# Kernel optimization log

Measured on AMD Instinct MI355X. Metric: run time of the kernel, lower is better.

Reference implementation:

```python
import jax, jax.numpy as jnp
import numpy as np

VOCAB, VEC, HID, ATT, DOM, B, S = 50000, 300, 256, 500, 16, 64, 128


def _gru_scan(gi_all, h0, Whh, bhh):
    # gi_all: [S,B,3H] precomputed input projections; returns hs: [S,B,H]
    def step(h, gi):
        gh = h @ Whh.T + bhh
        i_r, i_z, i_n = jnp.split(gi, 3, axis=-1)
        h_r, h_z, h_n = jnp.split(gh, 3, axis=-1)
        r = jax.nn.sigmoid(i_r + h_r)
        zg = jax.nn.sigmoid(i_z + h_z)
        n = jnp.tanh(i_n + r * h_n)
        h_new = (1.0 - zg) * n + zg * h
        return h_new, h_new
    _, hs = jax.lax.scan(step, h0, gi_all)
    return hs


def setup_inputs() -> dict:
    key = jax.random.key(0)
    ks = jax.random.split(key, 16)
    def xavier(k, shape):
        fan_in, fan_out = shape[-1], shape[0]
        std = float(np.sqrt(2.0 / (fan_in + fan_out)))
        return jax.random.normal(k, shape, dtype=jnp.float32) * std
    inp = {
        'x': jax.random.randint(ks[0], (B, S), 0, VOCAB),
        'z': jax.random.randint(ks[1], (B,), 0, DOM),
        'emb': jax.random.normal(ks[2], (VOCAB, VEC), dtype=jnp.float32) * 0.1,
        'Wih_f': xavier(ks[3], (3 * HID, VEC)),
        'Whh_f': xavier(ks[4], (3 * HID, HID)),
        'bih_f': jnp.zeros((3 * HID,), jnp.float32),
        'bhh_f': jnp.zeros((3 * HID,), jnp.float32),
        'Wih_b': xavier(ks[5], (3 * HID, VEC)),
        'Whh_b': xavier(ks[6], (3 * HID, HID)),
        'bih_b': jnp.zeros((3 * HID,), jnp.float32),
        'bhh_b': jnp.zeros((3 * HID,), jnp.float32),
        'att_fc_W': xavier(ks[7], (ATT, 2 * HID)),
        'att_fc_b': jnp.zeros((ATT,), jnp.float32),
        'att_weight': xavier(ks[8], (DOM, ATT)),
        'fc_W': xavier(ks[9], (2, 2 * HID)),
        'fc_b': jnp.zeros((2,), jnp.float32),
    }
    return inp


def reference(x, z, emb, Wih_f, Whh_f, bih_f, bhh_f, Wih_b, Whh_b, bih_b, bhh_b,
              att_fc_W, att_fc_b, att_weight, fc_W, fc_b):
    xe = emb[x]                              # [B,S,VEC]
    xs = jnp.transpose(xe, (1, 0, 2))        # [S,B,VEC] (seq-major like torch GRU)
    h0 = jnp.zeros((x.shape[0], HID), jnp.float32)
    gi_f = jnp.einsum('sbv,gv->sbg', xs, Wih_f) + bih_f
    hs_f = _gru_scan(gi_f, h0, Whh_f, bhh_f)                       # [S,B,H]
    gi_b = jnp.einsum('sbv,gv->sbg', xs[::-1], Wih_b) + bih_b
    hs_b = _gru_scan(gi_b, h0, Whh_b, bhh_b)[::-1]                 # [S,B,H]
    h = jnp.transpose(jnp.concatenate([hs_f, hs_b], axis=-1), (1, 0, 2))  # [B,S,2H]
    hr = jnp.tanh(jnp.einsum('bsh,ah->bsa', h, att_fc_W) + att_fc_b)      # [B,S,ATT]
    # batched gather of per-domain attention vector, then per-row dot
    u = jnp.einsum('bsa,ba->bs', hr, att_weight[z])                        # [B,S]
    att = jax.nn.softmax(u, axis=1)                                        # [B,S]
    pooled = jnp.einsum('bsh,bs->bh', h, att)                              # [B,2H]
    # dropout is identity in eval mode
    return pooled @ fc_W.T + fc_b                                          # [B,2]
```

## Files before the change

kernel.cpp:

```cpp
#include <hip/hip_runtime.h>
#include <math.h>

#define VEC   300
#define HID   256
#define ATT   500
#define NB    64
#define NS    128
#define G3    768
#define GIC   1536
#define H2    512

typedef _Float16 half1;
typedef _Float16 h2_t  __attribute__((ext_vector_type(2)));
typedef _Float16 h4_t  __attribute__((ext_vector_type(4)));
typedef _Float16 f16x8 __attribute__((ext_vector_type(8)));
typedef float    f32x4 __attribute__((ext_vector_type(4)));

#if __has_builtin(__builtin_amdgcn_exp2f)
#define EXP2F(x) __builtin_amdgcn_exp2f(x)
#else
#define EXP2F(x) exp2f(x)
#endif
#if __has_builtin(__builtin_amdgcn_rcpf)
#define RCPF(x) __builtin_amdgcn_rcpf(x)
#else
#define RCPF(x) (1.0f/(x))
#endif

__device__ __forceinline__ float sigm(float x){ return RCPF(1.f + EXP2F(-1.44269504f*x)); }
__device__ __forceinline__ float tanh_fast(float x){ return 1.f - 2.f*RCPF(1.f + EXP2F(2.88539008f*x)); }

#if __has_builtin(__builtin_amdgcn_fdot2)
#define FDOT(w,h,acc) __builtin_amdgcn_fdot2((w),(h),(acc),false)
#else
#define FDOT(w,h,acc) ((acc) + (float)(w).x*(float)(h).x + (float)(w).y*(float)(h).y)
#endif

__global__ __launch_bounds__(256) void k_prep(const float* __restrict__ Wf,
                       const float* __restrict__ Wb, h2_t* __restrict__ Wpk){
  int o = blockIdx.x*256 + threadIdx.x;
  int t = o & 1023;
  int rest = o >> 10;
  int j = rest % 3;
  int p = (rest/3) & 31;
  int dir = rest / 96;
  int u = t & 255, ks = t >> 8;
  const float* W = dir ? Wb : Wf;
  int k0 = ks*64 + 2*p;
  h2_t w;
  w.x = (half1)W[(j*HID+u)*HID + k0];
  w.y = (half1)W[(j*HID+u)*HID + k0 + 1];
  Wpk[o] = w;
}

__global__ __launch_bounds__(256) void k_prepA(const float* __restrict__ afW,
                       half1* __restrict__ afW16){
  int o = blockIdx.x*256 + threadIdx.x;
  int n = o >> 9, k = o & 511;
  afW16[o] = (half1)((n < ATT) ? afW[n*H2 + k] : 0.f);
}

__global__ __launch_bounds__(256)
__attribute__((amdgpu_waves_per_eu(4, 4)))
void k_gi_mfma(const int* __restrict__ x,
      const float* __restrict__ emb,
      const float* __restrict__ Wf, const float* __restrict__ Wb,
      const float* __restrict__ bf, const float* __restrict__ bb,
      float* __restrict__ gi){
  __shared__ half1 Al[128*40];
  __shared__ half1 Bl[128*40];
  __shared__ int   xi[128];
  const int t = threadIdx.x;
  const int row0 = blockIdx.x * 128;
  const int col0 = blockIdx.y * 128;
  if (t < 128) {
    int i = row0 + t; int s = i >> 6; int b = i & 63;
    xi[t] = x[b*NS + s];
  }
  __syncthreads();

  const int lane = t & 63, wid = t >> 6;
  const int wr = wid >> 1, wc = wid & 1;
  const int l15 = lane & 15, lk = lane >> 4;

  f32x4 acc[4][4];
#pragma unroll
  for (int i = 0; i < 4; ++i)
#pragma unroll
    for (int j = 0; j < 4; ++j) acc[i][j] = (f32x4){0.f,0.f,0.f,0.f};

  for (int ks = 0; ks < 10; ++ks) {
#pragma unroll
    for (int l = 0; l < 8; ++l) {
      int idx = l*256 + t;
      int row = idx >> 4;
      int kp  = idx & 15;
      int kk  = ks*32 + kp*2;
      h2_t va; va.x = (half1)0.f; va.y = (half1)0.f;
      h2_t vb; vb.x = (half1)0.f; vb.y = (half1)0.f;
      if (kk < VEC) {
        float2 e = *reinterpret_cast<const float2*>(&emb[(long)xi[row]*VEC + kk]);
        va.x = (half1)e.x; va.y = (half1)e.y;
        int g = col0 + row;
        const float* W = (g < G3) ? &Wf[(long)g*VEC] : &Wb[(long)(g-G3)*VEC];
        float2 w2 = *reinterpret_cast<const float2*>(&W[kk]);
        vb.x = (half1)w2.x; vb.y = (half1)w2.y;
      }
      *reinterpret_cast<h2_t*>(&Al[row*40 + kp*2]) = va;
      *reinterpret_cast<h2_t*>(&Bl[row*40 + kp*2]) = vb;
    }
    __syncthreads();
    f16x8 af[4], bfq[4];
#pragma unroll
    for (int i = 0; i < 4; ++i)
      af[i]  = *reinterpret_cast<const f16x8*>(&Al[(wr*64 + i*16 + l15)*40 + lk*8]);
#pragma unroll
    for (int j = 0; j < 4; ++j)
      bfq[j] = *reinterpret_cast<const f16x8*>(&Bl[(wc*64 + j*16 + l15)*40 + lk*8]);
#pragma unroll
    for (int i = 0; i < 4; ++i)
#pragma unroll
      for (int j = 0; j < 4; ++j)
        acc[i][j] = __builtin_amdgcn_mfma_f32_16x16x32_f16(af[i], bfq[j], acc[i][j], 0, 0, 0);
    __syncthreads();
  }

#pragma unroll
  for (int j = 0; j < 4; ++j) {
    int gcol = col0 + wc*64 + j*16 + l15;
    float bj = (gcol < G3) ? bf[gcol] : bb[gcol - G3];
#pragma unroll
    for (int i = 0; i < 4; ++i) {
      int grow0 = row0 + wr*64 + i*16 + lk*4;
#pragma unroll
      for (int q = 0; q < 4; ++q)
        gi[(long)(grow0 + q)*GIC + gcol] = acc[i][j][q] + bj;
    }
  }
}

#define RP2(M) M(0,1) M(2,3) M(4,5) M(6,7) M(8,9) M(10,11) M(12,13) M(14,15) \
               M(16,17) M(18,19) M(20,21) M(22,23)
#define RPL(M) M(0) M(1) M(2) M(3) M(4) M(5) M(6) M(7) M(8) M(9) M(10) M(11) \
               M(12) M(13) M(14) M(15) M(16) M(17) M(18) M(19) M(20) M(21) M(22) M(23)

__global__ __launch_bounds__(1024)
__attribute__((amdgpu_waves_per_eu(4, 4)))
void k_scan_reg(const float* __restrict__ gi,
     const h2_t* __restrict__ Wpk,
     const float* __restrict__ bhf, const float* __restrict__ bhb,
     float* __restrict__ hseq){
  __shared__ half1 hl16[264];
  __shared__ float part[256*13];
  __shared__ h2_t  lds_w[24*1024];
  const int t   = threadIdx.x;
  const int u   = t & 255;
  const int ks  = t >> 8;
  const int kb  = ks * 64;
  const int dir = blockIdx.x & 1;
  const int b   = blockIdx.x >> 1;
  const float* bhh = dir ? bhb : bhf;
  const h2_t* wp = Wpk + (long)dir*96*1024 + t;

#define DECLW(p) h2_t wA##p, wB##p, wC##p;
  RPL(DECLW)
#define LOADW(p) wA##p = wp[((p)*3+0)*1024]; wB##p = wp[((p)*3+1)*1024]; wC##p = wp[((p)*3+2)*1024];
  RPL(LOADW)
#pragma unroll
  for (int q = 0; q < 24; ++q)
    lds_w[q*1024 + t] = wp[(72+q)*1024];

  float bh0=0.f, bh1=0.f, bh2=0.f;
  if (ks == 0) { bh0 = bhh[u]; bh1 = bhh[HID+u]; bh2 = bhh[2*HID+u]; }
  if (t < 256) hl16[t] = (half1)0.f;
  float hprev = 0.f;
  __syncthreads();

#pragma unroll 1
  for (int tt = 0; tt < NS; ++tt) {
    const int s = dir ? (NS-1-tt) : tt;
    float i0=0.f, i1=0.f, i2=0.f;
    if (ks == 0) {
      long base = ((long)s*NB + b)*GIC + dir*G3 + u;
      i0 = gi[base]; i1 = gi[base+HID]; i2 = gi[base+2*HID];
    }
    float a0=0.f, a1=0.f, a2=0.f;
#define FMAW2(pa,pb) { h4_t hh4 = *reinterpret_cast<const h4_t*>(&hl16[kb + 2*(pa)]); \
    h2_t lo; lo.x = hh4.x; lo.y = hh4.y; \
    h2_t hi; hi.x = hh4.z; hi.y = hh4.w; \
    a0 = FDOT(wA##pa, lo, a0); a1 = FDOT(wB##pa, lo, a1); a2 = FDOT(wC##pa, lo, a2); \
    a0 = FDOT(wA##pb, hi, a0); a1 = FDOT(wB##pb, hi, a1); a2 = FDOT(wC##pb, hi, a2); }
    RP2(FMAW2)
#pragma unroll
    for (int q = 0; q < 4; ++q) {
      h4_t hh4 = *reinterpret_cast<const h4_t*>(&hl16[kb + 48 + 4*q]);
      h2_t lo; lo.x = hh4.x; lo.y = hh4.y;
      h2_t hi; hi.x = hh4.z; hi.y = hh4.w;
      h2_t w0a = lds_w[((2*q)*3+0)*1024 + t];
      h2_t w1a = lds_w[((2*q)*3+1)*1024 + t];
      h2_t w2a = lds_w[((2*q)*3+2)*1024 + t];
      h2_t w0b = lds_w[((2*q+1)*3+0)*1024 + t];
      h2_t w1b = lds_w[((2*q+1)*3+1)*1024 + t];
      h2_t w2b = lds_w[((2*q+1)*3+2)*1024 + t];
      a0 = FDOT(w0a, lo, a0); a1 = FDOT(w1a, lo, a1); a2 = FDOT(w2a, lo, a2);
      a0 = FDOT(w0b, hi, a0); a1 = FDOT(w1b, hi, a1); a2 = FDOT(w2b, hi, a2);
    }
    part[u*13 + ks*3 + 0] = a0;
    part[u*13 + ks*3 + 1] = a1;
    part[u*13 + ks*3 + 2] = a2;
    __syncthreads();
    if (ks == 0) {
      float g0 = bh0 + part[u*13+0] + part[u*13+3] + part[u*13+6] + part[u*13+9];
      float g1 = bh1 + part[u*13+1] + part[u*13+4] + part[u*13+7] + part[u*13+10];
      float g2 = bh2 + part[u*13+2] + part[u*13+5] + part[u*13+8] + part[u*13+11];
      float r  = sigm(i0 + g0);
      float zg = sigm(i1 + g1);
      float n  = tanh_fast(i2 + r*g2);
      float hn = (1.f - zg)*n + zg*hprev;
      hprev = hn;
      hl16[u] = (half1)hn;
      hseq[((long)b*NS + s)*H2 + dir*HID + u] = hn;
    }
    __syncthreads();
  }
}

__global__ __launch_bounds__(256)
__attribute__((amdgpu_waves_per_eu(4, 4)))
void k_att1_mfma(const float* __restrict__ hseq, const half1* __restrict__ afW16,
    const float* __restrict__ afb, const float* __restrict__ attw,
    const int* __restrict__ z, float* __restrict__ ub){
  __shared__ half1 Ah[32*520];
  __shared__ float red[4*32];
  const int t  = threadIdx.x;
  const int b  = blockIdx.x;
  const int s0 = blockIdx.y * 32;
  const int lane = t & 63, w = t >> 6;
  const int l15 = lane & 15, lk = lane >> 4;

#pragma unroll
  for (int l = 0; l < 64; ++l) {
    int idx = l*256 + t;
    int sl = idx >> 9, c = idx & 511;
    Ah[sl*520 + c] = (half1)hseq[((long)b*NS + s0 + sl)*H2 + c];
  }
  __syncthreads();

  f32x4 acc[2][8];
#pragma unroll
  for (int i = 0; i < 2; ++i)
#pragma unroll
    for (int j = 0; j < 8; ++j) acc[i][j] = (f32x4){0.f,0.f,0.f,0.f};

#pragma unroll 2
  for (int ksn = 0; ksn < 16; ++ksn) {
    f16x8 af[2];
#pragma unroll
    for (int mt = 0; mt < 2; ++mt)
      af[mt] = *reinterpret_cast<const f16x8*>(&Ah[(mt*16 + l15)*520 + ksn*32 + lk*8]);
#pragma unroll
    for (int nt = 0; nt < 8; ++nt) {
      int n = w*128 + nt*16 + l15;
      f16x8 bf = *reinterpret_cast<const f16x8*>(&afW16[(long)n*512 + ksn*32 + lk*8]);
#pragma unroll
      for (int mt = 0; mt < 2; ++mt)
        acc[mt][nt] = __builtin_amdgcn_mfma_f32_16x16x32_f16(af[mt], bf, acc[mt][nt], 0, 0, 0);
    }
  }

  float us[8];
#pragma unroll
  for (int i = 0; i < 8; ++i) us[i] = 0.f;
  const int zb = z[b];
#pragma unroll
  for (int nt = 0; nt < 8; ++nt) {
    int n = w*128 + nt*16 + l15;
    float ab = (n < ATT) ? afb[n] : 0.f;
    float aw = (n < ATT) ? attw[zb*ATT + n] : 0.f;
#pragma unroll
    for (int mt = 0; mt < 2; ++mt)
#pragma unroll
      for (int q = 0; q < 4; ++q)
        us[mt*4+q] += tanh_fast(acc[mt][nt][q] + ab) * aw;
  }
#pragma unroll
  for (int off = 1; off < 16; off <<= 1)
#pragma unroll
    for (int i = 0; i < 8; ++i) us[i] += __shfl_xor(us[i], off, 64);
  if (l15 == 0) {
#pragma unroll
    for (int i = 0; i < 8; ++i) {
      int row = (i >> 2)*16 + lk*4 + (i & 3);
      red[w*32 + row] = us[i];
    }
  }
  __syncthreads();
  if (t < 32)
    ub[b*NS + s0 + t] = red[t] + red[32+t] + red[64+t] + red[96+t];
}

__global__ __launch_bounds__(256) void k_att2(const float* __restrict__ hseq,
   const float* __restrict__ ub, const float* __restrict__ fcW,
   const float* __restrict__ fcb, float* __restrict__ out){
  __shared__ float att[NS];
  __shared__ float red[256];
  __shared__ float pool[H2];
  const int t = threadIdx.x, b = blockIdx.x;
  float v = (t < NS) ? ub[b*NS + t] : -3.4e38f;
  red[t] = v; __syncthreads();
  for (int off = 128; off >= 1; off >>= 1) {
    if (t < off) red[t] = fmaxf(red[t], red[t+off]);
    __syncthreads();
  }
  float mx = red[0]; __syncthreads();
  float e = (t < NS) ? EXP2F(1.44269504f*(v - mx)) : 0.f;
  red[t] = e; __syncthreads();
  for (int off = 128; off >= 1; off >>= 1) {
    if (t < off) red[t] += red[t+off];
    __syncthreads();
  }
  float sm = red[0]; __syncthreads();
  if (t < NS) att[t] = e / sm;
  __syncthreads();
#pragma unroll
  for (int rep = 0; rep < 2; ++rep) {
    int c = rep*256 + t;
    float acc = 0.f;
#pragma unroll 4
    for (int s = 0; s < NS; ++s) acc += att[s] * hseq[((long)b*NS + s)*H2 + c];
    pool[c] = acc;
  }
  __syncthreads();
  for (int j = 0; j < 2; ++j) {
    float p = pool[t]*fcW[j*H2+t] + pool[t+256]*fcW[j*H2+t+256];
    red[t] = p; __syncthreads();
    for (int off = 128; off >= 1; off >>= 1) {
      if (t < off) red[t] += red[t+off];
      __syncthreads();
    }
    if (t == 0) out[b*2+j] = red[0] + fcb[j];
    __syncthreads();
  }
}

extern "C" void kernel_launch(void* const* d_in, const int* in_sizes, int n_in,
                              void* d_out, int out_size, void* d_ws, size_t ws_size,
                              hipStream_t stream) {
  const int*   x     = (const int*)  d_in[0];
  const int*   z     = (const int*)  d_in[1];
  const float* emb   = (const float*)d_in[2];
  const float* Wih_f = (const float*)d_in[3];
  const float* Whh_f = (const float*)d_in[4];
  const float* bih_f = (const float*)d_in[5];
  const float* bhh_f = (const float*)d_in[6];
  const float* Wih_b = (const float*)d_in[7];
  const float* Whh_b = (const float*)d_in[8];
  const float* bih_b = (const float*)d_in[9];
  const float* bhh_b = (const float*)d_in[10];
  const float* afW   = (const float*)d_in[11];
  const float* afb   = (const float*)d_in[12];
  const float* attw  = (const float*)d_in[13];
  const float* fcW   = (const float*)d_in[14];
  const float* fcb   = (const float*)d_in[15];

  float* ws    = (float*)d_ws;
  h2_t*  Wpk   = (h2_t*)ws;
  half1* afW16 = (half1*)(ws + 196608);
  float* giW   = ws   + 196608 + 131072;
  float* hseq  = giW  + 12582912;
  float* ubuf  = hseq + 4194304;

  k_prep <<<dim3(768),  dim3(256), 0, stream>>>(Whh_f, Whh_b, Wpk);
  k_prepA<<<dim3(1024), dim3(256), 0, stream>>>(afW, afW16);
  k_gi_mfma<<<dim3(64,12), dim3(256), 0, stream>>>(x, emb, Wih_f, Wih_b, bih_f, bih_b, giW);
  k_scan_reg<<<dim3(128), dim3(1024), 0, stream>>>(giW, Wpk, bhh_f, bhh_b, hseq);
  k_att1_mfma<<<dim3(64,4), dim3(256), 0, stream>>>(hseq, afW16, afb, attw, z, ubuf);
  k_att2<<<dim3(64), dim3(256), 0, stream>>>(hseq, ubuf, fcW, fcb, (float*)d_out);
}
```

Measured before the change: 247.0 us.

## Hold full recurrent weights in registers with 512-thread GRU scan blocks

New measurement: 233.8 us. 1.06x faster.

```diff
diff --git a/kernel.cpp b/kernel.cpp
--- a/kernel.cpp
+++ b/kernel.cpp
@@ -12,9 +12,10 @@
 
 typedef _Float16 half1;
 typedef _Float16 h2_t  __attribute__((ext_vector_type(2)));
-typedef _Float16 h4_t  __attribute__((ext_vector_type(4)));
 typedef _Float16 f16x8 __attribute__((ext_vector_type(8)));
 typedef float    f32x4 __attribute__((ext_vector_type(4)));
+
+struct __align__(16) H8 { h2_t a, b, c, d; };
 
 #if __has_builtin(__builtin_amdgcn_exp2f)
 #define EXP2F(x) __builtin_amdgcn_exp2f(x)
@@ -139,36 +140,43 @@
   }
 }
 
-#define RP2(M) M(0,1) M(2,3) M(4,5) M(6,7) M(8,9) M(10,11) M(12,13) M(14,15) \
-               M(16,17) M(18,19) M(20,21) M(22,23)
-#define RPL(M) M(0) M(1) M(2) M(3) M(4) M(5) M(6) M(7) M(8) M(9) M(10) M(11) \
-               M(12) M(13) M(14) M(15) M(16) M(17) M(18) M(19) M(20) M(21) M(22) M(23)
-
-__global__ __launch_bounds__(1024)
-__attribute__((amdgpu_waves_per_eu(4, 4)))
-void k_scan_reg(const float* __restrict__ gi,
+#define DECL12(X,g,UNUSED) h2_t X##g##a0,X##g##a1,X##g##a2, X##g##b0,X##g##b1,X##g##b2, \
+                                X##g##c0,X##g##c1,X##g##c2, X##g##d0,X##g##d1,X##g##d2;
+#define LOAD12(X,g,WP) \
+  X##g##a0=(WP)[((4*(g)+0)*3+0)*1024]; X##g##a1=(WP)[((4*(g)+0)*3+1)*1024]; X##g##a2=(WP)[((4*(g)+0)*3+2)*1024]; \
+  X##g##b0=(WP)[((4*(g)+1)*3+0)*1024]; X##g##b1=(WP)[((4*(g)+1)*3+1)*1024]; X##g##b2=(WP)[((4*(g)+1)*3+2)*1024]; \
+  X##g##c0=(WP)[((4*(g)+2)*3+0)*1024]; X##g##c1=(WP)[((4*(g)+2)*3+1)*1024]; X##g##c2=(WP)[((4*(g)+2)*3+2)*1024]; \
+  X##g##d0=(WP)[((4*(g)+3)*3+0)*1024]; X##g##d1=(WP)[((4*(g)+3)*3+1)*1024]; X##g##d2=(WP)[((4*(g)+3)*3+2)*1024];
+#define FMA12(X,g,BOFF) { \
+  H8 hv = *reinterpret_cast<const H8*>(&hl16[kb + (BOFF) + (g)*8]); \
+  a0=FDOT(X##g##a0,hv.a,a0); a1=FDOT(X##g##a1,hv.a,a1); a2=FDOT(X##g##a2,hv.a,a2); \
+  a0=FDOT(X##g##b0,hv.b,a0); a1=FDOT(X##g##b1,hv.b,a1); a2=FDOT(X##g##b2,hv.b,a2); \
+  a0=FDOT(X##g##c0,hv.c,a0); a1=FDOT(X##g##c1,hv.c,a1); a2=FDOT(X##g##c2,hv.c,a2); \
+  a0=FDOT(X##g##d0,hv.d,a0); a1=FDOT(X##g##d1,hv.d,a1); a2=FDOT(X##g##d2,hv.d,a2); }
+#define GRP8(M,X,A2) M(X,0,A2) M(X,1,A2) M(X,2,A2) M(X,3,A2) M(X,4,A2) M(X,5,A2) M(X,6,A2) M(X,7,A2)
+
+__global__ __launch_bounds__(512)
+__attribute__((amdgpu_waves_per_eu(2, 2)))
+void k_scan_reg2(const float* __restrict__ gi,
      const h2_t* __restrict__ Wpk,
      const float* __restrict__ bhf, const float* __restrict__ bhb,
      float* __restrict__ hseq){
-  __shared__ half1 hl16[264];
-  __shared__ float part[256*13];
-  __shared__ h2_t  lds_w[24*1024];
+  __shared__ __align__(16) half1 hl16[264];
+  __shared__ float part[3*256];
   const int t   = threadIdx.x;
   const int u   = t & 255;
   const int ks  = t >> 8;
-  const int kb  = ks * 64;
+  const int kb  = ks * 128;
   const int dir = blockIdx.x & 1;
   const int b   = blockIdx.x >> 1;
   const float* bhh = dir ? bhb : bhf;
-  const h2_t* wp = Wpk + (long)dir*96*1024 + t;
-
-#define DECLW(p) h2_t wA##p, wB##p, wC##p;
-  RPL(DECLW)
-#define LOADW(p) wA##p = wp[((p)*3+0)*1024]; wB##p = wp[((p)*3+1)*1024]; wC##p = wp[((p)*3+2)*1024];
-  RPL(LOADW)
-#pragma unroll
-  for (int q = 0; q < 24; ++q)
-    lds_w[q*1024 + t] = wp[(72+q)*1024];
+  const h2_t* wpA = Wpk + (long)dir*96*1024 + (2*ks)*256 + u;
+  const h2_t* wpB = Wpk + (long)dir*96*1024 + (2*ks+1)*256 + u;
+
+  GRP8(DECL12, A, 0)
+  GRP8(DECL12, B, 0)
+  GRP8(LOAD12, A, wpA)
+  GRP8(LOAD12, B, wpB)
 
   float bh0=0.f, bh1=0.f, bh2=0.f;
   if (ks == 0) { bh0 = bhh[u]; bh1 = bhh[HID+u]; bh2 = bhh[2*HID+u]; }
@@ -185,34 +193,14 @@
       i0 = gi[base]; i1 = gi[base+HID]; i2 = gi[base+2*HID];
     }
     float a0=0.f, a1=0.f, a2=0.f;
-#define FMAW2(pa,pb) { h4_t hh4 = *reinterpret_cast<const h4_t*>(&hl16[kb + 2*(pa)]); \
-    h2_t lo; lo.x = hh4.x; lo.y = hh4.y; \
-    h2_t hi; hi.x = hh4.z; hi.y = hh4.w; \
-    a0 = FDOT(wA##pa, lo, a0); a1 = FDOT(wB##pa, lo, a1); a2 = FDOT(wC##pa, lo, a2); \
-    a0 = FDOT(wA##pb, hi, a0); a1 = FDOT(wB##pb, hi, a1); a2 = FDOT(wC##pb, hi, a2); }
-    RP2(FMAW2)
-#pragma unroll
-    for (int q = 0; q < 4; ++q) {
-      h4_t hh4 = *reinterpret_cast<const h4_t*>(&hl16[kb + 48 + 4*q]);
-      h2_t lo; lo.x = hh4.x; lo.y = hh4.y;
-      h2_t hi; hi.x = hh4.z; hi.y = hh4.w;
-      h2_t w0a = lds_w[((2*q)*3+0)*1024 + t];
-      h2_t w1a = lds_w[((2*q)*3+1)*1024 + t];
-      h2_t w2a = lds_w[((2*q)*3+2)*1024 + t];
-      h2_t w0b = lds_w[((2*q+1)*3+0)*1024 + t];
-      h2_t w1b = lds_w[((2*q+1)*3+1)*1024 + t];
-      h2_t w2b = lds_w[((2*q+1)*3+2)*1024 + t];
-      a0 = FDOT(w0a, lo, a0); a1 = FDOT(w1a, lo, a1); a2 = FDOT(w2a, lo, a2);
-      a0 = FDOT(w0b, hi, a0); a1 = FDOT(w1b, hi, a1); a2 = FDOT(w2b, hi, a2);
-    }
-    part[u*13 + ks*3 + 0] = a0;
-    part[u*13 + ks*3 + 1] = a1;
-    part[u*13 + ks*3 + 2] = a2;
+    GRP8(FMA12, A, 0)
+    GRP8(FMA12, B, 64)
+    if (ks == 1) { part[u] = a0; part[256+u] = a1; part[512+u] = a2; }
     __syncthreads();
     if (ks == 0) {
-      float g0 = bh0 + part[u*13+0] + part[u*13+3] + part[u*13+6] + part[u*13+9];
-      float g1 = bh1 + part[u*13+1] + part[u*13+4] + part[u*13+7] + part[u*13+10];
-      float g2 = bh2 + part[u*13+2] + part[u*13+5] + part[u*13+8] + part[u*13+11];
+      float g0 = bh0 + a0 + part[u];
+      float g1 = bh1 + a1 + part[256+u];
+      float g2 = bh2 + a2 + part[512+u];
       float r  = sigm(i0 + g0);
       float zg = sigm(i1 + g1);
       float n  = tanh_fast(i2 + r*g2);
@@ -373,7 +361,7 @@
   k_prep <<<dim3(768),  dim3(256), 0, stream>>>(Whh_f, Whh_b, Wpk);
   k_prepA<<<dim3(1024), dim3(256), 0, stream>>>(afW, afW16);
   k_gi_mfma<<<dim3(64,12), dim3(256), 0, stream>>>(x, emb, Wih_f, Wih_b, bih_f, bih_b, giW);
-  k_scan_reg<<<dim3(128), dim3(1024), 0, stream>>>(giW, Wpk, bhh_f, bhh_b, hseq);
+  k_scan_reg2<<<dim3(128), dim3(512), 0, stream>>>(giW, Wpk, bhh_f, bhh_b, hseq);
   k_att1_mfma<<<dim3(64,4), dim3(256), 0, stream>>>(hseq, afW16, afb, attw, z, ubuf);
   k_att2<<<dim3(64), dim3(256), 0, stream>>>(hseq, ubuf, fcW, fcb, (float*)d_out);
 }
```
